# Kernel tuning notes

Measured on AMD Instinct MI355X. Metric: run time of the kernel, lower is better.

## Reference

```python
import jax, jax.numpy as jnp
import numpy as np

N = 50000      # nodes
E = 1600000    # edges (avg degree 32)
D = 256        # in_dim
H = 256        # hid
L = 3          # num_layers (all layer input dims equal D==H)
EPS_LN = 1e-5  # torch LayerNorm default eps
EPS_DEN = 1e-8 # denom clamp from the module


def setup_inputs() -> dict:
    key = jax.random.key(0)
    ks = jax.random.split(key, 6)
    x = jax.random.normal(ks[0], (N, D), dtype=jnp.float32)
    edge_index = jax.random.randint(ks[1], (2, E), 0, N, dtype=jnp.int32)
    # stacked per-layer params (all layers share dims since in_dim == hid)
    W_sage = jax.random.normal(ks[2], (L, 2 * D, H), dtype=jnp.float32) * 0.02
    b_sage = jnp.zeros((L, H), dtype=jnp.float32)
    gamma = jnp.ones((L, H), dtype=jnp.float32)
    beta = jnp.zeros((L, H), dtype=jnp.float32)
    W_attn = jax.random.normal(ks[3], (L, 2 * D), dtype=jnp.float32) * 0.02
    b_attn = jnp.zeros((L,), dtype=jnp.float32)
    W_skip = jax.random.normal(ks[4], (D, H), dtype=jnp.float32) * 0.02
    b_skip = jnp.zeros((H,), dtype=jnp.float32)
    return {"x": x, "edge_index": edge_index, "W_sage": W_sage, "b_sage": b_sage,
            "gamma": gamma, "beta": beta, "W_attn": W_attn, "b_attn": b_attn,
            "W_skip": W_skip, "b_skip": b_skip}


def reference(x, edge_index, W_sage, b_sage, gamma, beta, W_attn, b_attn, W_skip, b_skip):
    src, dst = edge_index[0], edge_index[1]
    residual = x @ W_skip + b_skip  # (N, H)
    h = x
    for i in range(L):
        d = h.shape[1]
        # edge attention: attn_lin(cat([x[dst], x[src]])) == (x@w_dst)[dst] + (x@w_src)[src] + b
        w = W_attn[i]
        s_dst = h @ w[:d]          # (N,)
        s_src = h @ w[d:]          # (N,)
        raw = s_dst[dst] + s_src[src] + b_attn[i]   # (E,)
        a = jnp.exp(raw)
        denom = jax.ops.segment_sum(a, dst, num_segments=N)        # (N,)
        alpha = a / jnp.maximum(denom[dst], EPS_DEN)               # (E,)
        agg = jax.ops.segment_sum(alpha[:, None] * h[src], dst, num_segments=N)  # (N, d)
        # SAGE linear on cat([h, agg]) + LayerNorm + ReLU
        z = jnp.concatenate([h, agg], axis=-1) @ W_sage[i] + b_sage[i]  # (N, H)
        mu = z.mean(axis=-1, keepdims=True)
        var = z.var(axis=-1, keepdims=True)
        h = jax.nn.relu(gamma[i] * (z - mu) / jnp.sqrt(var + EPS_LN) + beta[i])
    return (h + residual).mean(axis=0)  # (H,)
```

## Files before the change

kernel.cpp:

```cpp
#include <hip/hip_runtime.h>
#include <hip/hip_bf16.h>

#define NN 50000
#define EE 1600000
#define DIM 256
#define KDIM 512
#define NLAYER 3
#define NRANGE 8
#define RNODES (NN / NRANGE)
#define CAP 80

using bf16x8 = __attribute__((ext_vector_type(8))) short;
using f32x4  = __attribute__((ext_vector_type(4))) float;
using f32x2  = __attribute__((ext_vector_type(2))) float;

static __device__ __forceinline__ unsigned short f2bf(float f) {
    unsigned u = __builtin_bit_cast(unsigned, f);
    unsigned r = (u + 0x7FFFu + ((u >> 16) & 1u)) >> 16;
    return (unsigned short)r;
}
static __device__ __forceinline__ float bf2f(unsigned short s) {
    return __builtin_bit_cast(float, (unsigned)s << 16);
}

static __device__ __forceinline__ void gload_lds16(const void* g, void* l) {
    __builtin_amdgcn_global_load_lds(
        reinterpret_cast<const __attribute__((address_space(1))) void*>(
            reinterpret_cast<uintptr_t>(g)),
        reinterpret_cast<__attribute__((address_space(3))) void*>(
            static_cast<unsigned>(reinterpret_cast<uintptr_t>(l))),
        16, 0, 0);
}

#if defined(__has_builtin) && __has_builtin(__builtin_amdgcn_cvt_pk_f32_fp8) && __has_builtin(__builtin_amdgcn_cvt_pk_fp8_f32)
#define FP8_NATIVE 1
#else
#define FP8_NATIVE 0
#endif

template <bool HI>
static __device__ __forceinline__ f32x2 fp8x2_dec(unsigned w) {
#if FP8_NATIVE
    return __builtin_amdgcn_cvt_pk_f32_fp8((int)w, HI);
#else
    unsigned v = HI ? (w >> 16) : w;
    unsigned b0 = v & 0xFFu, b1 = (v >> 8) & 0xFFu;
    unsigned u0 = ((b0 & 0x80u) << 24) | ((b0 & 0x7Fu) << 20);
    unsigned u1 = ((b1 & 0x80u) << 24) | ((b1 & 0x7Fu) << 20);
    f32x2 r;
    r[0] = __builtin_bit_cast(float, u0) * 0x1p120f;
    r[1] = __builtin_bit_cast(float, u1) * 0x1p120f;
    return r;
#endif
}

#if !FP8_NATIVE
static __device__ __forceinline__ unsigned fp8_enc1(float f) {
    unsigned u = __builtin_bit_cast(unsigned, f * 0x1p-120f);
    unsigned s = (u >> 24) & 0x80u;
    unsigned m = u & 0x7FFFFFFFu;
    m = m + 0x7FFFFu + ((m >> 20) & 1u);
    return s | ((m >> 20) & 0x7Fu);
}
#endif

static __device__ __forceinline__ unsigned fp8x4_enc(float a, float b, float c, float d) {
#if FP8_NATIVE
    int w = __builtin_amdgcn_cvt_pk_fp8_f32(a, b, 0, false);
    w = __builtin_amdgcn_cvt_pk_fp8_f32(c, d, w, true);
    return (unsigned)w;
#else
    return fp8_enc1(a) | (fp8_enc1(b) << 8) | (fp8_enc1(c) << 16) | (fp8_enc1(d) << 24);
#endif
}

static __device__ __forceinline__ void fp8x8_fma(float* acc, unsigned lo, unsigned hi, float wg) {
    f32x2 p0 = fp8x2_dec<false>(lo);
    f32x2 p1 = fp8x2_dec<true>(lo);
    f32x2 p2 = fp8x2_dec<false>(hi);
    f32x2 p3 = fp8x2_dec<true>(hi);
    acc[0] += wg * p0[0]; acc[1] += wg * p0[1];
    acc[2] += wg * p1[0]; acc[3] += wg * p1[1];
    acc[4] += wg * p2[0]; acc[5] += wg * p2[1];
    acc[6] += wg * p3[0]; acc[7] += wg * p3[1];
}

static __device__ __forceinline__ void fp8x16_fma(float* acc, uint4 r, float wg) {
    fp8x8_fma(acc, r.x, r.y, wg);
    fp8x8_fma(acc + 8, r.z, r.w, wg);
}

__global__ __launch_bounds__(256) void k_prep(const float* __restrict__ x,
                                              const float* __restrict__ w_src,
                                              unsigned short* __restrict__ hout,
                                              unsigned char* __restrict__ f8out,
                                              float* __restrict__ e_src) {
    int wave = threadIdx.x >> 6, lane = threadIdx.x & 63;
    int n = blockIdx.x * 4 + wave;
    if (n >= NN) return;
    const float4 v = *reinterpret_cast<const float4*>(x + (size_t)n * DIM + lane * 4);
    const float4 wv = *reinterpret_cast<const float4*>(w_src + lane * 4);
    float sc = v.x * wv.x + v.y * wv.y + v.z * wv.z + v.w * wv.w;
    #pragma unroll
    for (int m = 32; m; m >>= 1) sc += __shfl_xor(sc, m);
    if (lane == 0) e_src[n] = __expf(sc);
    ushort4 o;
    o.x = f2bf(v.x); o.y = f2bf(v.y); o.z = f2bf(v.z); o.w = f2bf(v.w);
    *reinterpret_cast<ushort4*>(hout + (size_t)n * DIM + lane * 4) = o;
    *reinterpret_cast<unsigned*>(f8out + (size_t)n * DIM + lane * 4) =
        fp8x4_enc(v.x, v.y, v.z, v.w);
}

__global__ __launch_bounds__(256) void k_scatter(const int* __restrict__ ei, int* __restrict__ cursor,
                                                 unsigned short* __restrict__ csr) {
    const int range = blockIdx.x & (NRANGE - 1);
    const int lo = range * RNODES, hi = lo + RNODES;
    const int stride = (gridDim.x >> 3) * 256;
    for (int e = (blockIdx.x >> 3) * 256 + threadIdx.x; e < EE; e += stride) {
        int d = ei[EE + e];
        if (d >= lo && d < hi) {
            int pos = atomicAdd(&cursor[d], 1);
            if (pos < CAP) csr[d * CAP + pos] = (unsigned short)ei[e];
        }
    }
}

__global__ __launch_bounds__(256) void k_pad(int* __restrict__ cursor,
                                             unsigned short* __restrict__ csr) {
    int n = blockIdx.x * 256 + threadIdx.x;
    if (n >= NN) return;
    int deg = cursor[n];
    if (deg > CAP) deg = CAP;
    int padded = (deg + 15) & ~15;
    if (padded > CAP) padded = CAP;
    for (int p = deg; p < padded; ++p) csr[(size_t)n * CAP + p] = (unsigned short)NN;
    cursor[n] = padded;
}

__global__ __launch_bounds__(256) void k_aggregate(const unsigned char* __restrict__ f8,
                                                   const float* __restrict__ e_src,
                                                   const int* __restrict__ cursor,
                                                   const unsigned short* __restrict__ csr,
                                                   unsigned short* __restrict__ agg) {
    int wave = threadIdx.x >> 6, lane = threadIdx.x & 63;
    int n = blockIdx.x * 4 + wave;
    if (n >= NN) return;
    int deg = cursor[n];
    const unsigned short* row = csr + (size_t)n * CAP;
    const int g = lane >> 4;
    const int col16 = (lane & 15) * 16;

    float acc[16];
    #pragma unroll
    for (int j = 0; j < 16; ++j) acc[j] = 0.f;
    float den = 0.f;

    uint2 iw = make_uint2(0u, 0u);
    if (deg > 0) iw = *reinterpret_cast<const uint2*>(row + 4 * g);

    #pragma unroll 2
    for (int p = 0; p + 16 <= deg; p += 16) {
        int np = p + 16;
        uint2 iw_n = *reinterpret_cast<const uint2*>(
            row + ((np + 16 <= deg) ? np : 0) + 4 * g);
        int s0 = iw.x & 0xFFFF, s1 = iw.x >> 16;
        int s2 = iw.y & 0xFFFF, s3 = iw.y >> 16;
        float w0 = e_src[s0], w1 = e_src[s1], w2 = e_src[s2], w3 = e_src[s3];
        uint4 r0 = *reinterpret_cast<const uint4*>(f8 + (size_t)s0 * DIM + col16);
        uint4 r1 = *reinterpret_cast<const uint4*>(f8 + (size_t)s1 * DIM + col16);
        uint4 r2 = *reinterpret_cast<const uint4*>(f8 + (size_t)s2 * DIM + col16);
        uint4 r3 = *reinterpret_cast<const uint4*>(f8 + (size_t)s3 * DIM + col16);
        fp8x16_fma(acc, r0, w0);
        fp8x16_fma(acc, r1, w1);
        fp8x16_fma(acc, r2, w2);
        fp8x16_fma(acc, r3, w3);
        den += (w0 + w1) + (w2 + w3);
        iw = iw_n;
    }

    den += __shfl_xor(den, 16);
    den += __shfl_xor(den, 32);
    float inv = (den > 0.f) ? 1.f / den : 0.f;
    #pragma unroll
    for (int j = 0; j < 16; ++j) {
        acc[j] += __shfl_xor(acc[j], 16);
        acc[j] += __shfl_xor(acc[j], 32);
    }

    if (g == 0) {
        bf16x8 o0, o1;
        #pragma unroll
        for (int j = 0; j < 8; ++j) {
            o0[j] = (short)f2bf(acc[j] * inv);
            o1[j] = (short)f2bf(acc[j + 8] * inv);
        }
        *reinterpret_cast<bf16x8*>(agg + (size_t)n * DIM + col16) = o0;
        *reinterpret_cast<bf16x8*>(agg + (size_t)n * DIM + col16 + 8) = o1;
    }
}

__global__ __launch_bounds__(256) void k_packB(const float* __restrict__ W, unsigned short* __restrict__ Bp) {
    int tid = blockIdx.x * 256 + threadIdx.x;
    int j    = tid & 7;
    int lane = (tid >> 3) & 63;
    int nf   = (tid >> 9) & 15;
    int ks   = tid >> 13;
    int c = lane & 15, q = lane >> 4;
    Bp[tid] = f2bf(W[(size_t)(ks * 32 + q * 8 + j) * DIM + nf * 16 + c]);
}

#define LDS_STRIDE 264
__global__ __launch_bounds__(256) void k_gemm_ln(const unsigned short* __restrict__ hin,
                                                 const unsigned short* __restrict__ agg,
                                                 const unsigned short* __restrict__ Bp,
                                                 const float* __restrict__ bias,
                                                 const float* __restrict__ gamma_l,
                                                 const float* __restrict__ beta_l,
                                                 const float* __restrict__ w_src_next,
                                                 unsigned short* __restrict__ hout,
                                                 unsigned char* __restrict__ f8out,
                                                 float* __restrict__ e_src) {
    __shared__ __align__(16) unsigned char lds_raw[4 * 16 * LDS_STRIDE * 2];
    unsigned short* bbuf0 = (unsigned short*)lds_raw;
    unsigned short* bbuf1 = bbuf0 + 8192;
    int w = threadIdx.x >> 6, lane = threadIdx.x & 63;
    int c = lane & 15, q = lane >> 4;
    int m0 = blockIdx.x * 64 + w * 16;

    auto stage = [&](int ks, unsigned short* buf) {
        const unsigned short* g = Bp + (size_t)ks * 8192 + w * 2048 + lane * 8;
        unsigned short* l = buf + w * 2048;
        #pragma unroll
        for (int i = 0; i < 4; ++i)
            gload_lds16(g + i * 512, l + i * 512);
    };

    f32x4 acc[16];
    #pragma unroll
    for (int nf = 0; nf < 16; ++nf) {
        float b = bias[nf * 16 + c];
        acc[nf] = (f32x4){b, b, b, b};
    }

    stage(0, bbuf0);
    bf16x8 a_cur = *reinterpret_cast<const bf16x8*>(hin + (size_t)(m0 + c) * DIM + q * 8);
    __syncthreads();

    #pragma unroll
    for (int ks = 0; ks < 16; ++ks) {
        const unsigned short* bb = (ks & 1) ? bbuf1 : bbuf0;
        unsigned short* bnext    = (ks & 1) ? bbuf0 : bbuf1;
        bf16x8 a_next = a_cur;
        if (ks + 1 < 16) {
            stage(ks + 1, bnext);
            const int kk1 = (ks + 1) * 32;
            const unsigned short* hs = (kk1 < DIM) ? hin : agg;
            a_next = *reinterpret_cast<const bf16x8*>(
                hs + (size_t)(m0 + c) * DIM + (kk1 & (DIM - 1)) + q * 8);
        }
        #pragma unroll
        for (int nf = 0; nf < 16; ++nf) {
            bf16x8 bfr = *reinterpret_cast<const bf16x8*>(bb + nf * 512 + lane * 8);
            acc[nf] = __builtin_amdgcn_mfma_f32_16x16x32_bf16(a_cur, bfr, acc[nf], 0, 0, 0);
        }
        __syncthreads();
        a_cur = a_next;
    }

    #pragma unroll
    for (int r = 0; r < 4; ++r) {
        float s = 0.f, s2 = 0.f;
        #pragma unroll
        for (int nf = 0; nf < 16; ++nf) {
            float v = acc[nf][r];
            s += v; s2 += v * v;
        }
        #pragma unroll
        for (int msk = 1; msk < 16; msk <<= 1) {
            s  += __shfl_xor(s, msk);
            s2 += __shfl_xor(s2, msk);
        }
        float mu = s * (1.f / DIM);
        float var = s2 * (1.f / DIM) - mu * mu;
        float rstd = rsqrtf(var + 1e-5f);
        float sc = 0.f;
        #pragma unroll
        for (int nf = 0; nf < 16; ++nf) {
            float v = fmaxf(gamma_l[nf * 16 + c] * (acc[nf][r] - mu) * rstd + beta_l[nf * 16 + c], 0.f);
            acc[nf][r] = v;
            if (w_src_next) sc += v * w_src_next[nf * 16 + c];
        }
        if (w_src_next) {
            #pragma unroll
            for (int msk = 1; msk < 16; msk <<= 1) sc += __shfl_xor(sc, msk);
            int row = m0 + q * 4 + r;
            if (c == 0 && row < NN) e_src[row] = __expf(sc);
        }
    }

    unsigned short* myl = (unsigned short*)lds_raw + w * 16 * LDS_STRIDE;
    #pragma unroll
    for (int nf = 0; nf < 16; ++nf) {
        #pragma unroll
        for (int r = 0; r < 4; ++r)
            myl[(q * 4 + r) * LDS_STRIDE + nf * 16 + c] = f2bf(acc[nf][r]);
    }
    #pragma unroll
    for (int i = 0; i < 8; ++i) {
        int row16 = 2 * i + (lane >> 5);
        bf16x8 v = *reinterpret_cast<const bf16x8*>(myl + row16 * LDS_STRIDE + (lane & 31) * 8);
        int grow = m0 + row16;
        if (grow < NN) {
            *reinterpret_cast<bf16x8*>(hout + (size_t)grow * DIM + (lane & 31) * 8) = v;
            if (f8out) {
                uint2 pk;
                pk.x = fp8x4_enc(bf2f((unsigned short)v[0]), bf2f((unsigned short)v[1]),
                                 bf2f((unsigned short)v[2]), bf2f((unsigned short)v[3]));
                pk.y = fp8x4_enc(bf2f((unsigned short)v[4]), bf2f((unsigned short)v[5]),
                                 bf2f((unsigned short)v[6]), bf2f((unsigned short)v[7]));
                *reinterpret_cast<uint2*>(f8out + (size_t)grow * DIM + (lane & 31) * 8) = pk;
            }
        }
    }
}

__global__ __launch_bounds__(256) void k_colsum_f32(const float* __restrict__ mat, float* __restrict__ out) {
    int j = threadIdx.x;
    float s = 0.f;
    for (int r = blockIdx.x; r < NN; r += gridDim.x) s += mat[(size_t)r * DIM + j];
    atomicAdd(&out[j], s);
}
__global__ __launch_bounds__(256) void k_colsum_bf16(const unsigned short* __restrict__ mat,
                                                     float* __restrict__ out) {
    int j = threadIdx.x;
    float s = 0.f;
    for (int r = blockIdx.x; r < NN; r += gridDim.x) s += bf2f(mat[(size_t)r * DIM + j]);
    atomicAdd(&out[j], s);
}

__global__ __launch_bounds__(256) void k_final(const float* __restrict__ hsum, const float* __restrict__ xsum,
                                               const float* __restrict__ W_skip, const float* __restrict__ b_skip,
                                               float* __restrict__ out) {
    int j = threadIdx.x;
    float acc = 0.f;
    const float invN = 1.f / (float)NN;
    for (int i = 0; i < DIM; ++i) acc += (xsum[i] * invN) * W_skip[(size_t)i * DIM + j];
    out[j] = hsum[j] * invN + acc + b_skip[j];
}

extern "C" void kernel_launch(void* const* d_in, const int* in_sizes, int n_in,
                              void* d_out, int out_size, void* d_ws, size_t ws_size,
                              hipStream_t stream) {
    const float* x      = (const float*)d_in[0];
    const int*   ei     = (const int*)d_in[1];
    const float* W_sage = (const float*)d_in[2];
    const float* b_sage = (const float*)d_in[3];
    const float* gamma  = (const float*)d_in[4];
    const float* beta   = (const float*)d_in[5];
    const float* W_attn = (const float*)d_in[6];
    const float* W_skip = (const float*)d_in[8];
    const float* b_skip = (const float*)d_in[9];
    float* out = (float*)d_out;

    const size_t ND = (size_t)NN * DIM;
    unsigned short* hx   = (unsigned short*)d_ws;
    unsigned short* hA   = hx + ND;
    unsigned short* hB   = hA + ND;
    unsigned short* agg  = hB + ND;
    unsigned short* Bp   = agg + ND;
    unsigned char*  f8a  = (unsigned char*)(Bp + (size_t)KDIM * DIM + 64);
    unsigned char*  f8b  = f8a + ND + DIM;
    float* e_src  = (float*)(f8b + ND + DIM + 64);
    float* colsum = e_src + NN + 16;
    float* xsum   = colsum + DIM;
    int*   cursor = (int*)(xsum + DIM);
    unsigned short* csr = (unsigned short*)(cursor + NN);

    const int NBLK_RANGED = NRANGE * 784;
    const int NBLK_N = (NN + 255) / 256;

    hipError_t err;
    err = hipMemsetAsync(cursor, 0, (size_t)NN * sizeof(int), stream); (void)err;
    err = hipMemsetAsync(colsum, 0, 2 * DIM * sizeof(float), stream); (void)err;
    err = hipMemsetAsync(f8a + ND, 0, DIM, stream); (void)err;
    err = hipMemsetAsync(f8b + ND, 0, DIM, stream); (void)err;
    err = hipMemsetAsync(e_src + NN, 0, sizeof(float), stream); (void)err;

    k_scatter<<<NBLK_RANGED, 256, 0, stream>>>(ei, cursor, csr);
    k_pad<<<NBLK_N, 256, 0, stream>>>(cursor, csr);

    k_prep<<<NN / 4, 256, 0, stream>>>(x, W_attn + DIM, hx, f8a, e_src);

    unsigned short* hbufs[3] = {hx, hA, hB};
    unsigned char*  f8bufs[3] = {f8a, f8b, f8a};
    for (int l = 0; l < NLAYER; ++l) {
        unsigned short* h_in  = hbufs[l];
        unsigned short* h_out = hbufs[l + 1 < 3 ? l + 1 : 1];
        k_packB<<<(KDIM * DIM) / 256, 256, 0, stream>>>(W_sage + (size_t)l * KDIM * DIM, Bp);
        k_aggregate<<<NN / 4, 256, 0, stream>>>(f8bufs[l], e_src, cursor, csr, agg);
        const float* wnext = (l < NLAYER - 1) ? (W_attn + (size_t)(l + 1) * KDIM + DIM) : nullptr;
        unsigned char* f8next = (l < NLAYER - 1) ? f8bufs[l + 1] : nullptr;
        k_gemm_ln<<<(NN + 63) / 64, 256, 0, stream>>>(
            h_in, agg, Bp, b_sage + (size_t)l * DIM,
            gamma + (size_t)l * DIM, beta + (size_t)l * DIM,
            wnext, h_out, f8next, e_src);
    }

    k_colsum_bf16<<<256, 256, 0, stream>>>(hbufs[1], colsum);
    k_colsum_f32<<<256, 256, 0, stream>>>(x, xsum);
    k_final<<<1, 256, 0, stream>>>(colsum, xsum, W_skip, b_skip, out);
}
```

Baseline: 533.3 us.

## Fuse neighbor aggregation into GEMM+LayerNorm kernel and fold final column sum

Removes the standalone aggregation kernel. Each wave of the GEMM kernel first gathers and normalizes the 16 rows it will multiply, writes them to the agg buffer, then drains its stores before running the MFMA loop. The attention-weight vector is now double-buffered, because blocks write the next layer's weights while other blocks may still be reading the current ones. The last layer also sums its output columns from LDS with atomics, replacing the separate bf16 column-sum pass. This saves launches and one full pass over h, but the latency-bound gather now runs at much lower wave-level parallelism, since each wave handles 16 nodes one after another under the GEMM kernel's occupancy.

```diff
diff --git a/kernel.cpp b/kernel.cpp
--- a/kernel.cpp
+++ b/kernel.cpp
@@ -137,68 +137,6 @@
     cursor[n] = padded;
 }
 
-__global__ __launch_bounds__(256) void k_aggregate(const unsigned char* __restrict__ f8,
-                                                   const float* __restrict__ e_src,
-                                                   const int* __restrict__ cursor,
-                                                   const unsigned short* __restrict__ csr,
-                                                   unsigned short* __restrict__ agg) {
-    int wave = threadIdx.x >> 6, lane = threadIdx.x & 63;
-    int n = blockIdx.x * 4 + wave;
-    if (n >= NN) return;
-    int deg = cursor[n];
-    const unsigned short* row = csr + (size_t)n * CAP;
-    const int g = lane >> 4;
-    const int col16 = (lane & 15) * 16;
-
-    float acc[16];
-    #pragma unroll
-    for (int j = 0; j < 16; ++j) acc[j] = 0.f;
-    float den = 0.f;
-
-    uint2 iw = make_uint2(0u, 0u);
-    if (deg > 0) iw = *reinterpret_cast<const uint2*>(row + 4 * g);
-
-    #pragma unroll 2
-    for (int p = 0; p + 16 <= deg; p += 16) {
-        int np = p + 16;
-        uint2 iw_n = *reinterpret_cast<const uint2*>(
-            row + ((np + 16 <= deg) ? np : 0) + 4 * g);
-        int s0 = iw.x & 0xFFFF, s1 = iw.x >> 16;
-        int s2 = iw.y & 0xFFFF, s3 = iw.y >> 16;
-        float w0 = e_src[s0], w1 = e_src[s1], w2 = e_src[s2], w3 = e_src[s3];
-        uint4 r0 = *reinterpret_cast<const uint4*>(f8 + (size_t)s0 * DIM + col16);
-        uint4 r1 = *reinterpret_cast<const uint4*>(f8 + (size_t)s1 * DIM + col16);
-        uint4 r2 = *reinterpret_cast<const uint4*>(f8 + (size_t)s2 * DIM + col16);
-        uint4 r3 = *reinterpret_cast<const uint4*>(f8 + (size_t)s3 * DIM + col16);
-        fp8x16_fma(acc, r0, w0);
-        fp8x16_fma(acc, r1, w1);
-        fp8x16_fma(acc, r2, w2);
-        fp8x16_fma(acc, r3, w3);
-        den += (w0 + w1) + (w2 + w3);
-        iw = iw_n;
-    }
-
-    den += __shfl_xor(den, 16);
-    den += __shfl_xor(den, 32);
-    float inv = (den > 0.f) ? 1.f / den : 0.f;
-    #pragma unroll
-    for (int j = 0; j < 16; ++j) {
-        acc[j] += __shfl_xor(acc[j], 16);
-        acc[j] += __shfl_xor(acc[j], 32);
-    }
-
-    if (g == 0) {
-        bf16x8 o0, o1;
-        #pragma unroll
-        for (int j = 0; j < 8; ++j) {
-            o0[j] = (short)f2bf(acc[j] * inv);
-            o1[j] = (short)f2bf(acc[j + 8] * inv);
-        }
-        *reinterpret_cast<bf16x8*>(agg + (size_t)n * DIM + col16) = o0;
-        *reinterpret_cast<bf16x8*>(agg + (size_t)n * DIM + col16 + 8) = o1;
-    }
-}
-
 __global__ __launch_bounds__(256) void k_packB(const float* __restrict__ W, unsigned short* __restrict__ Bp) {
     int tid = blockIdx.x * 256 + threadIdx.x;
     int j    = tid & 7;
@@ -210,22 +148,87 @@
 }
 
 #define LDS_STRIDE 264
-__global__ __launch_bounds__(256) void k_gemm_ln(const unsigned short* __restrict__ hin,
-                                                 const unsigned short* __restrict__ agg,
-                                                 const unsigned short* __restrict__ Bp,
-                                                 const float* __restrict__ bias,
-                                                 const float* __restrict__ gamma_l,
-                                                 const float* __restrict__ beta_l,
-                                                 const float* __restrict__ w_src_next,
-                                                 unsigned short* __restrict__ hout,
-                                                 unsigned char* __restrict__ f8out,
-                                                 float* __restrict__ e_src) {
+__global__ __launch_bounds__(256) void k_agg_gemm(const unsigned char* __restrict__ f8,
+                                                  const float* __restrict__ e_in,
+                                                  const int* __restrict__ cursor,
+                                                  const unsigned short* __restrict__ csr,
+                                                  unsigned short* __restrict__ aggbuf,
+                                                  const unsigned short* __restrict__ hin,
+                                                  const unsigned short* __restrict__ Bp,
+                                                  const float* __restrict__ bias,
+                                                  const float* __restrict__ gamma_l,
+                                                  const float* __restrict__ beta_l,
+                                                  const float* __restrict__ w_src_next,
+                                                  unsigned short* __restrict__ hout,
+                                                  unsigned char* __restrict__ f8out,
+                                                  float* __restrict__ e_out,
+                                                  float* __restrict__ colsum) {
     __shared__ __align__(16) unsigned char lds_raw[4 * 16 * LDS_STRIDE * 2];
     unsigned short* bbuf0 = (unsigned short*)lds_raw;
     unsigned short* bbuf1 = bbuf0 + 8192;
     int w = threadIdx.x >> 6, lane = threadIdx.x & 63;
     int c = lane & 15, q = lane >> 4;
     int m0 = blockIdx.x * 64 + w * 16;
+
+    {
+        const int g16 = lane >> 4;
+        const int col16 = (lane & 15) * 16;
+        for (int i = 0; i < 16; ++i) {
+            int n = m0 + i;
+            if (n >= NN) break;
+            int deg = cursor[n];
+            const unsigned short* row = csr + (size_t)n * CAP;
+
+            float acc[16];
+            #pragma unroll
+            for (int j = 0; j < 16; ++j) acc[j] = 0.f;
+            float den = 0.f;
+
+            uint2 iw = make_uint2(0u, 0u);
+            if (deg > 0) iw = *reinterpret_cast<const uint2*>(row + 4 * g16);
+
+            #pragma unroll 2
+            for (int p = 0; p + 16 <= deg; p += 16) {
+                int np = p + 16;
+                uint2 iw_n = *reinterpret_cast<const uint2*>(
+                    row + ((np + 16 <= deg) ? np : 0) + 4 * g16);
+                int s0 = iw.x & 0xFFFF, s1 = iw.x >> 16;
+                int s2 = iw.y & 0xFFFF, s3 = iw.y >> 16;
+                float w0 = e_in[s0], w1 = e_in[s1], w2 = e_in[s2], w3 = e_in[s3];
+                uint4 r0 = *reinterpret_cast<const uint4*>(f8 + (size_t)s0 * DIM + col16);
+                uint4 r1 = *reinterpret_cast<const uint4*>(f8 + (size_t)s1 * DIM + col16);
+                uint4 r2 = *reinterpret_cast<const uint4*>(f8 + (size_t)s2 * DIM + col16);
+                uint4 r3 = *reinterpret_cast<const uint4*>(f8 + (size_t)s3 * DIM + col16);
+                fp8x16_fma(acc, r0, w0);
+                fp8x16_fma(acc, r1, w1);
+                fp8x16_fma(acc, r2, w2);
+                fp8x16_fma(acc, r3, w3);
+                den += (w0 + w1) + (w2 + w3);
+                iw = iw_n;
+            }
+
+            den += __shfl_xor(den, 16);
+            den += __shfl_xor(den, 32);
+            float inv = (den > 0.f) ? 1.f / den : 0.f;
+            #pragma unroll
+            for (int j = 0; j < 16; ++j) {
+                acc[j] += __shfl_xor(acc[j], 16);
+                acc[j] += __shfl_xor(acc[j], 32);
+            }
+
+            if (g16 == 0) {
+                bf16x8 o0, o1;
+                #pragma unroll
+                for (int j = 0; j < 8; ++j) {
+                    o0[j] = (short)f2bf(acc[j] * inv);
+                    o1[j] = (short)f2bf(acc[j + 8] * inv);
+                }
+                *reinterpret_cast<bf16x8*>(aggbuf + (size_t)n * DIM + col16) = o0;
+                *reinterpret_cast<bf16x8*>(aggbuf + (size_t)n * DIM + col16 + 8) = o1;
+            }
+        }
+        asm volatile("s_waitcnt vmcnt(0)" ::: "memory");
+    }
 
     auto stage = [&](int ks, unsigned short* buf) {
         const unsigned short* g = Bp + (size_t)ks * 8192 + w * 2048 + lane * 8;
@@ -254,7 +257,7 @@
         if (ks + 1 < 16) {
             stage(ks + 1, bnext);
             const int kk1 = (ks + 1) * 32;
-            const unsigned short* hs = (kk1 < DIM) ? hin : agg;
+            const unsigned short* hs = (kk1 < DIM) ? hin : aggbuf;
             a_next = *reinterpret_cast<const bf16x8*>(
                 hs + (size_t)(m0 + c) * DIM + (kk1 & (DIM - 1)) + q * 8);
         }
@@ -294,7 +297,7 @@
             #pragma unroll
             for (int msk = 1; msk < 16; msk <<= 1) sc += __shfl_xor(sc, msk);
             int row = m0 + q * 4 + r;
-            if (c == 0 && row < NN) e_src[row] = __expf(sc);
+            if (c == 0 && row < NN) e_out[row] = __expf(sc);
         }
     }
 
@@ -322,19 +325,25 @@
             }
         }
     }
+
+    if (colsum) {
+        __syncthreads();
+        int t = threadIdx.x;
+        float s = 0.f;
+        unsigned short* l0 = (unsigned short*)lds_raw;
+        #pragma unroll 4
+        for (int r = 0; r < 64; ++r) {
+            if (blockIdx.x * 64 + r < NN)
+                s += bf2f(l0[((r >> 4) * 16 + (r & 15)) * LDS_STRIDE + t]);
+        }
+        atomicAdd(&colsum[t], s);
+    }
 }
 
 __global__ __launch_bounds__(256) void k_colsum_f32(const float* __restrict__ mat, float* __restrict__ out) {
     int j = threadIdx.x;
     float s = 0.f;
     for (int r = blockIdx.x; r < NN; r += gridDim.x) s += mat[(size_t)r * DIM + j];
-    atomicAdd(&out[j], s);
-}
-__global__ __launch_bounds__(256) void k_colsum_bf16(const unsigned short* __restrict__ mat,
-                                                     float* __restrict__ out) {
-    int j = threadIdx.x;
-    float s = 0.f;
-    for (int r = blockIdx.x; r < NN; r += gridDim.x) s += bf2f(mat[(size_t)r * DIM + j]);
     atomicAdd(&out[j], s);
 }
 
@@ -370,43 +379,47 @@
     unsigned short* Bp   = agg + ND;
     unsigned char*  f8a  = (unsigned char*)(Bp + (size_t)KDIM * DIM + 64);
     unsigned char*  f8b  = f8a + ND + DIM;
-    float* e_src  = (float*)(f8b + ND + DIM + 64);
-    float* colsum = e_src + NN + 16;
+    float* e_a    = (float*)(f8b + ND + DIM + 64);
+    float* e_b    = e_a + NN + 16;
+    float* colsum = e_b + NN + 16;
     float* xsum   = colsum + DIM;
     int*   cursor = (int*)(xsum + DIM);
     unsigned short* csr = (unsigned short*)(cursor + NN);
 
     const int NBLK_RANGED = NRANGE * 784;
     const int NBLK_N = (NN + 255) / 256;
+    const int NBLK_G = (NN + 63) / 64;
 
     hipError_t err;
     err = hipMemsetAsync(cursor, 0, (size_t)NN * sizeof(int), stream); (void)err;
     err = hipMemsetAsync(colsum, 0, 2 * DIM * sizeof(float), stream); (void)err;
     err = hipMemsetAsync(f8a + ND, 0, DIM, stream); (void)err;
     err = hipMemsetAsync(f8b + ND, 0, DIM, stream); (void)err;
-    err = hipMemsetAsync(e_src + NN, 0, sizeof(float), stream); (void)err;
+    err = hipMemsetAsync(e_a + NN, 0, sizeof(float), stream); (void)err;
+    err = hipMemsetAsync(e_b + NN, 0, sizeof(float), stream); (void)err;
 
     k_scatter<<<NBLK_RANGED, 256, 0, stream>>>(ei, cursor, csr);
     k_pad<<<NBLK_N, 256, 0, stream>>>(cursor, csr);
 
-    k_prep<<<NN / 4, 256, 0, stream>>>(x, W_attn + DIM, hx, f8a, e_src);
-
-    unsigned short* hbufs[3] = {hx, hA, hB};
+    k_prep<<<NN / 4, 256, 0, stream>>>(x, W_attn + DIM, hx, f8a, e_a);
+
+    k_colsum_f32<<<256, 256, 0, stream>>>(x, xsum);
+
+    unsigned short* hbufs[4]  = {hx, hA, hB, hA};
     unsigned char*  f8bufs[3] = {f8a, f8b, f8a};
+    float*          ebufs[2]  = {e_a, e_b};
     for (int l = 0; l < NLAYER; ++l) {
-        unsigned short* h_in  = hbufs[l];
-        unsigned short* h_out = hbufs[l + 1 < 3 ? l + 1 : 1];
         k_packB<<<(KDIM * DIM) / 256, 256, 0, stream>>>(W_sage + (size_t)l * KDIM * DIM, Bp);
-        k_aggregate<<<NN / 4, 256, 0, stream>>>(f8bufs[l], e_src, cursor, csr, agg);
-        const float* wnext = (l < NLAYER - 1) ? (W_attn + (size_t)(l + 1) * KDIM + DIM) : nullptr;
-        unsigned char* f8next = (l < NLAYER - 1) ? f8bufs[l + 1] : nullptr;
-        k_gemm_ln<<<(NN + 63) / 64, 256, 0, stream>>>(
-            h_in, agg, Bp, b_sage + (size_t)l * DIM,
+        const bool last = (l == NLAYER - 1);
+        const float* wnext = last ? nullptr : (W_attn + (size_t)(l + 1) * KDIM + DIM);
+        unsigned char* f8next = last ? nullptr : f8bufs[l + 1];
+        k_agg_gemm<<<NBLK_G, 256, 0, stream>>>(
+            f8bufs[l], ebufs[l & 1], cursor, csr, agg,
+            hbufs[l], Bp, b_sage + (size_t)l * DIM,
             gamma + (size_t)l * DIM, beta + (size_t)l * DIM,
-            wnext, h_out, f8next, e_src);
-    }
-
-    k_colsum_bf16<<<256, 256, 0, stream>>>(hbufs[1], colsum);
-    k_colsum_f32<<<256, 256, 0, stream>>>(x, xsum);
+            wnext, hbufs[l + 1], f8next, ebufs[(l + 1) & 1],
+            last ? colsum : nullptr);
+    }
+
     k_final<<<1, 256, 0, stream>>>(colsum, xsum, W_skip, b_skip, out);
 }
```

Measured after the change: 562.4 us. 5.5% more time.
